# Kernel optimization log

Hardware: AMD Instinct MI355X
Metric: run time of the kernel (lower is better)

Reference implementation:

```python
import jax, jax.numpy as jnp
import numpy as np

N, E, H, C = 50000, 800000, 4, 32   # nodes, edges, heads, per-head channels
HID, LAT, G = H * C, 32, 128        # hidden, latent, num graphs
IN_DIM = 64
NEG_SLOPE = 0.2
BN_EPS = 1e-5


def setup_inputs() -> dict:
    key = jax.random.key(0)
    ks = jax.random.split(key, 20)
    inp = {
        "x": jax.random.normal(ks[0], (N, IN_DIM), jnp.float32),
        "edge_index": jax.random.randint(ks[1], (2, E), 0, N, jnp.int32),
        "batch": jnp.sort(jax.random.randint(ks[2], (N,), 0, G, jnp.int32)),
        # layer 0
        "W0": jax.random.normal(ks[3], (IN_DIM, HID), jnp.float32) * (1.0 / np.sqrt(IN_DIM)),
        "a_src0": jax.random.normal(ks[4], (H, C), jnp.float32) * 0.1,
        "a_dst0": jax.random.normal(ks[5], (H, C), jnp.float32) * 0.1,
        "b0": jnp.zeros((HID,), jnp.float32),
        # layer 1
        "W1": jax.random.normal(ks[6], (HID, HID), jnp.float32) * (1.0 / np.sqrt(HID)),
        "a_src1": jax.random.normal(ks[7], (H, C), jnp.float32) * 0.1,
        "a_dst1": jax.random.normal(ks[8], (H, C), jnp.float32) * 0.1,
        "b1": jnp.zeros((HID,), jnp.float32),
        # layer 2
        "W2": jax.random.normal(ks[9], (HID, HID), jnp.float32) * (1.0 / np.sqrt(HID)),
        "a_src2": jax.random.normal(ks[10], (H, C), jnp.float32) * 0.1,
        "a_dst2": jax.random.normal(ks[11], (H, C), jnp.float32) * 0.1,
        "b2": jnp.zeros((HID,), jnp.float32),
        # head
        "fc_w": jax.random.normal(ks[12], (HID, LAT), jnp.float32) * (1.0 / np.sqrt(HID)),
        "fc_b": jnp.zeros((LAT,), jnp.float32),
        "bn_g": jnp.ones((LAT,), jnp.float32),
        "bn_b": jnp.zeros((LAT,), jnp.float32),
    }
    return inp


def _gat_conv(x, src, dst, W, a_src, a_dst, b):
    n = x.shape[0]
    h = (x @ W).reshape(n, H, C)                      # [N,H,C]
    alpha_s = jnp.einsum("nhc,hc->nh", h, a_src)       # [N,H]
    alpha_d = jnp.einsum("nhc,hc->nh", h, a_dst)
    e = jax.nn.leaky_relu(alpha_s[src] + alpha_d[dst], NEG_SLOPE)  # [E',H]
    # scatter-softmax over incoming edges of each dst node
    m = jax.ops.segment_max(e, dst, num_segments=n)
    m = jnp.where(jnp.isfinite(m), m, 0.0)
    ex = jnp.exp(e - m[dst])
    denom = jax.ops.segment_sum(ex, dst, num_segments=n)
    alpha = ex / (denom[dst] + 1e-16)                  # [E',H]
    out = jax.ops.segment_sum(alpha[:, :, None] * h[src], dst, num_segments=n)
    return out.reshape(n, H * C) + b


def reference(x, edge_index, batch, W0, a_src0, a_dst0, b0, W1, a_src1, a_dst1, b1,
              W2, a_src2, a_dst2, b2, fc_w, fc_b, bn_g, bn_b):
    # PyG GATConv default add_self_loops=True
    loop = jnp.arange(N, dtype=edge_index.dtype)
    src = jnp.concatenate([edge_index[0], loop])
    dst = jnp.concatenate([edge_index[1], loop])

    h = x
    for (W, a_s, a_d, b) in ((W0, a_src0, a_dst0, b0),
                             (W1, a_src1, a_dst1, b1),
                             (W2, a_src2, a_dst2, b2)):
        h = _gat_conv(h, src, dst, W, a_s, a_d, b)
        h = jax.nn.leaky_relu(h, NEG_SLOPE)  # dropout is identity in eval

    pooled = jax.ops.segment_sum(h, batch, num_segments=G)  # global_add_pool -> [G,HID]
    out = pooled @ fc_w + fc_b
    # BatchNorm1d in eval mode with running_mean=0, running_var=1
    out = bn_g * out * (1.0 / np.sqrt(1.0 + BN_EPS)) + bn_b
    return out
```

## Files before the change

### kernel.cpp

```cpp
#include <hip/hip_runtime.h>
#include <hip/hip_bf16.h>
#include <float.h>

#define NEG 0.2f

__device__ __forceinline__ float leaky(float x) { return x > 0.0f ? x : NEG * x; }

__device__ __forceinline__ unsigned short f2bf(float f) {
  unsigned x = __float_as_uint(f);
  unsigned r = (x + 0x7fffu + ((x >> 16) & 1u)) >> 16;
  return (unsigned short)r;
}

__device__ __forceinline__ float2 bf2f2(unsigned u) {
  float2 r;
  r.x = __uint_as_float(u << 16);
  r.y = __uint_as_float(u & 0xffff0000u);
  return r;
}

using frag8 = __attribute__((ext_vector_type(8))) short;
using f32x4v = __attribute__((ext_vector_type(4))) float;

__global__ void zero_kernel(int* __restrict__ p, int n) {
  int i = blockIdx.x * blockDim.x + threadIdx.x;
  int stride = gridDim.x * blockDim.x;
  for (; i < n; i += stride) p[i] = 0;
}

__global__ void xcvt_kernel(const float* __restrict__ x, unsigned short* __restrict__ xb, int n) {
  int i = blockIdx.x * blockDim.x + threadIdx.x;
  if (i < n) xb[i] = f2bf(x[i]);
}

__global__ void count_kernel(const int* __restrict__ ei, int* __restrict__ deg, int E, int N) {
  int i = blockIdx.x * blockDim.x + threadIdx.x;
  if (i >= E + N) return;
  int dst = (i < E) ? ei[E + i] : (i - E);
  atomicAdd(&deg[dst], 1);
}

__global__ __launch_bounds__(1024) void scan_block_kernel(const int* __restrict__ deg,
                                                          int* __restrict__ row_start,
                                                          int* __restrict__ sums, int n) {
  __shared__ int buf[1024];
  int t = threadIdx.x;
  int idx = blockIdx.x * 1024 + t;
  int x = (idx < n) ? deg[idx] : 0;
  int v = x;
  buf[t] = v;
  __syncthreads();
  for (int off = 1; off < 1024; off <<= 1) {
    int a = (t >= off) ? buf[t - off] : 0;
    __syncthreads();
    v += a;
    buf[t] = v;
    __syncthreads();
  }
  if (idx < n) row_start[idx] = v - x;
  if (t == 1023) sums[blockIdx.x] = v;
}

__global__ __launch_bounds__(1024) void scan_sums_kernel(int* __restrict__ sums,
                                                         int* __restrict__ row_start,
                                                         int nch, int n) {
  __shared__ int buf[1024];
  int t = threadIdx.x;
  int x = (t < nch) ? sums[t] : 0;
  int v = x;
  buf[t] = v;
  __syncthreads();
  for (int off = 1; off < 1024; off <<= 1) {
    int a = (t >= off) ? buf[t - off] : 0;
    __syncthreads();
    v += a;
    buf[t] = v;
    __syncthreads();
  }
  if (t < nch) sums[t] = v - x;
  if (t == 1023) row_start[n] = v;
}

__global__ __launch_bounds__(1024) void scan_add_kernel(int* __restrict__ row_start,
                                                        const int* __restrict__ sums, int n) {
  int idx = blockIdx.x * 1024 + threadIdx.x;
  if (idx < n) row_start[idx] += sums[blockIdx.x];
}

__global__ void fill_kernel(const int* __restrict__ ei, int* __restrict__ cursor,
                            const int* __restrict__ row_start, int* __restrict__ csr_src,
                            int* __restrict__ csr_dst, int E, int N, int rpass) {
  int i = blockIdx.x * blockDim.x + threadIdx.x;
  if (i >= E + N) return;
  int src, dst;
  if (i < E) { src = ei[i]; dst = ei[E + i]; } else { src = dst = i - E; }
  if ((src >> 13) != rpass) return;
  int pos = atomicAdd(&cursor[dst], 1);
  int slot = row_start[dst] + pos;
  csr_src[slot] = src;
  csr_dst[slot] = dst;
}

__global__ __launch_bounds__(256) void gemm_kernel(const unsigned short* __restrict__ Xb,
                                                   const float* __restrict__ W,
                                                   unsigned short* __restrict__ Hb,
                                                   const float* __restrict__ a_src,
                                                   const float* __restrict__ a_dst,
                                                   float* __restrict__ as_arr,
                                                   float* __restrict__ ad_arr,
                                                   int nrows, int K) {
  __shared__ unsigned short Wt[128][136];
  __shared__ unsigned short Xs[64][136];
  int t = threadIdx.x;
  int wave = t >> 6, lane = t & 63;
  int n0 = lane & 15, quad = lane >> 4;
  int row0 = blockIdx.x * 64, wrow = wave * 16;

  for (int idx = t; idx < K * 128; idx += 256) {
    int k = idx >> 7, n = idx & 127;
    Wt[n][k] = f2bf(W[idx]);
  }
  int rowElems = K >> 3;
  for (int idx = t; idx < 64 * rowElems; idx += 256) {
    int r = idx / rowElems, c8 = idx % rowElems;
    int gr = row0 + r;
    uint4 v = make_uint4(0, 0, 0, 0);
    if (gr < nrows) v = *(const uint4*)(Xb + (size_t)gr * K + c8 * 8);
    *(uint4*)(&Xs[r][c8 * 8]) = v;
  }
  __syncthreads();

  f32x4v acc[8];
#pragma unroll
  for (int c = 0; c < 8; ++c) acc[c] = (f32x4v){0.f, 0.f, 0.f, 0.f};

  for (int kb = 0; kb < K; kb += 32) {
    frag8 a = *(const frag8*)(&Xs[wrow + n0][kb + quad * 8]);
#pragma unroll
    for (int c = 0; c < 8; ++c) {
      frag8 b = *(const frag8*)(&Wt[c * 16 + n0][kb + quad * 8]);
      acc[c] = __builtin_amdgcn_mfma_f32_16x16x32_bf16(a, b, acc[c], 0, 0, 0);
    }
  }

  float asv[8], adv[8];
#pragma unroll
  for (int c = 0; c < 8; ++c) {
    asv[c] = a_src[c * 16 + n0];
    adv[c] = a_dst[c * 16 + n0];
  }
#pragma unroll
  for (int r = 0; r < 4; ++r) {
    float ps[4] = {0.f, 0.f, 0.f, 0.f}, pd[4] = {0.f, 0.f, 0.f, 0.f};
#pragma unroll
    for (int c = 0; c < 8; ++c) {
      int h = c >> 1;
      ps[h] += acc[c][r] * asv[c];
      pd[h] += acc[c][r] * adv[c];
    }
#pragma unroll
    for (int off = 1; off < 16; off <<= 1) {
#pragma unroll
      for (int h = 0; h < 4; ++h) {
        ps[h] += __shfl_xor(ps[h], off);
        pd[h] += __shfl_xor(pd[h], off);
      }
    }
    if (n0 == 0) {
      int m = row0 + wrow + quad * 4 + r;
      if (m < nrows) {
#pragma unroll
        for (int h = 0; h < 4; ++h) {
          as_arr[(size_t)m * 4 + h] = ps[h];
          ad_arr[(size_t)m * 4 + h] = pd[h];
        }
      }
    }
  }

  __syncthreads();
#pragma unroll
  for (int c = 0; c < 8; ++c)
#pragma unroll
    for (int r = 0; r < 4; ++r)
      Xs[wrow + quad * 4 + r][c * 16 + n0] = f2bf(acc[c][r]);
  __syncthreads();
  for (int idx = t; idx < 64 * 16; idx += 256) {
    int r = idx >> 4, c8 = idx & 15;
    int gr = row0 + r;
    if (gr < nrows)
      *(uint4*)(Hb + (size_t)gr * 128 + c8 * 8) = *(const uint4*)(&Xs[r][c8 * 8]);
  }
}

__global__ __launch_bounds__(256) void ecomp_kernel(const int* __restrict__ csr_src,
                                                    const int* __restrict__ csr_dst,
                                                    const float* __restrict__ as_arr,
                                                    const float* __restrict__ ad_arr,
                                                    float* __restrict__ earr, int Etot) {
  int i = blockIdx.x * 256 + threadIdx.x;
  if (i >= Etot) return;
  int s = csr_src[i];
  int d = csr_dst[i];
  float4 a = *(const float4*)(as_arr + (size_t)s * 4);
  float4 b = *(const float4*)(ad_arr + (size_t)d * 4);
  float4 e;
  e.x = __expf(fminf(leaky(a.x + b.x), 80.f));
  e.y = __expf(fminf(leaky(a.y + b.y), 80.f));
  e.z = __expf(fminf(leaky(a.z + b.z), 80.f));
  e.w = __expf(fminf(leaky(a.w + b.w), 80.f));
  *(float4*)(earr + (size_t)i * 4) = e;
}

template <int POOL>
__global__ __launch_bounds__(256) void agg_kernel(const unsigned short* __restrict__ Hb,
                                                  const float* __restrict__ earr,
                                                  const int* __restrict__ csr_src,
                                                  const int* __restrict__ row_start,
                                                  const float* __restrict__ bias,
                                                  unsigned short* __restrict__ xnext,
                                                  const int* __restrict__ batch,
                                                  float* __restrict__ pooled, int N) {
  int wid = threadIdx.x >> 6;
  int lane = threadIdx.x & 63;
  int n = blockIdx.x * 4 + wid;
  if (n >= N) return;
  int rs = row_start[n], re = row_start[n + 1];
  int head = lane >> 4;

  const unsigned* hp = (const unsigned*)Hb + lane;
  const float* ep = earr + head;
  float denom = 0.f, acc0 = 0.f, acc1 = 0.f;
  int i = rs;
  for (; i + 4 <= re; i += 4) {
    int s0 = csr_src[i], s1 = csr_src[i + 1], s2 = csr_src[i + 2], s3 = csr_src[i + 3];
    float e0 = ep[(size_t)i * 4];
    float e1 = ep[(size_t)(i + 1) * 4];
    float e2 = ep[(size_t)(i + 2) * 4];
    float e3 = ep[(size_t)(i + 3) * 4];
    unsigned u0 = hp[(size_t)s0 * 64];
    unsigned u1 = hp[(size_t)s1 * 64];
    unsigned u2 = hp[(size_t)s2 * 64];
    unsigned u3 = hp[(size_t)s3 * 64];
    denom += (e0 + e1) + (e2 + e3);
    float2 f;
    f = bf2f2(u0); acc0 += e0 * f.x; acc1 += e0 * f.y;
    f = bf2f2(u1); acc0 += e1 * f.x; acc1 += e1 * f.y;
    f = bf2f2(u2); acc0 += e2 * f.x; acc1 += e2 * f.y;
    f = bf2f2(u3); acc0 += e3 * f.x; acc1 += e3 * f.y;
  }
  for (; i < re; ++i) {
    int s0 = csr_src[i];
    float e0 = ep[(size_t)i * 4];
    unsigned u0 = hp[(size_t)s0 * 64];
    float2 f = bf2f2(u0);
    denom += e0;
    acc0 += e0 * f.x;
    acc1 += e0 * f.y;
  }
  float inv = 1.0f / (denom + 1e-16f);
  float2 bv = *(const float2*)(bias + 2 * lane);
  float v0 = leaky(acc0 * inv + bv.x);
  float v1 = leaky(acc1 * inv + bv.y);
  if (POOL) {
    int g = batch[n];
    atomicAdd(&pooled[(size_t)g * 128 + 2 * lane], v0);
    atomicAdd(&pooled[(size_t)g * 128 + 2 * lane + 1], v1);
  } else {
    unsigned pk = ((unsigned)f2bf(v1) << 16) | (unsigned)f2bf(v0);
    ((unsigned*)xnext)[(size_t)n * 64 + lane] = pk;
  }
}

__global__ void head_kernel(const float* __restrict__ pooled, const float* __restrict__ fc_w,
                            const float* __restrict__ fc_b, const float* __restrict__ bn_g,
                            const float* __restrict__ bn_b, float* __restrict__ out, int G) {
  int t = threadIdx.x;
  int g = blockIdx.x * 8 + (t >> 5);
  int j = t & 31;
  if (g >= G) return;
  const float* pr = pooled + (size_t)g * 128;
  float acc = 0.f;
#pragma unroll 8
  for (int k = 0; k < 128; ++k) acc += pr[k] * fc_w[k * 32 + j];
  const float inv = 0.9999950000374997f;
  out[g * 32 + j] = bn_g[j] * (acc + fc_b[j]) * inv + bn_b[j];
}

extern "C" void kernel_launch(void* const* d_in, const int* in_sizes, int n_in,
                              void* d_out, int out_size, void* d_ws, size_t ws_size,
                              hipStream_t stream) {
  const float* x = (const float*)d_in[0];
  const int* ei = (const int*)d_in[1];
  const int* batch = (const int*)d_in[2];
  const float* Wm[3] = {(const float*)d_in[3], (const float*)d_in[7], (const float*)d_in[11]};
  const float* a_s[3] = {(const float*)d_in[4], (const float*)d_in[8], (const float*)d_in[12]};
  const float* a_d[3] = {(const float*)d_in[5], (const float*)d_in[9], (const float*)d_in[13]};
  const float* bb[3] = {(const float*)d_in[6], (const float*)d_in[10], (const float*)d_in[14]};
  const float* fc_w = (const float*)d_in[15];
  const float* fc_b = (const float*)d_in[16];
  const float* bn_g = (const float*)d_in[17];
  const float* bn_b = (const float*)d_in[18];
  float* out = (float*)d_out;

  int N = in_sizes[0] / 64;
  int E = in_sizes[1] / 2;
  int G = out_size / 32;
  int Etot = E + N;

  char* p = (char*)d_ws;
  auto carve = [&](size_t bytes) {
    char* r = p;
    p += (bytes + 255) & ~size_t(255);
    return r;
  };
  int* deg       = (int*)carve((size_t)N * 4);
  int* cursor    = (int*)carve((size_t)N * 4);
  float* pooled  = (float*)carve((size_t)G * 128 * 4);
  int* row_start = (int*)carve((size_t)(N + 1) * 4);
  int* sums      = (int*)carve(4096);
  int* csr_src   = (int*)carve((size_t)Etot * 4);
  int* csr_dst   = (int*)carve((size_t)Etot * 4);
  float* earr    = (float*)carve((size_t)Etot * 4 * 4);
  unsigned short* Hb = (unsigned short*)carve((size_t)N * 128 * 2);
  unsigned short* Xb = (unsigned short*)carve((size_t)N * 128 * 2);
  float* as_arr  = (float*)carve((size_t)N * 4 * 4);
  float* ad_arr  = (float*)carve((size_t)N * 4 * 4);

  int nz = (int)(((char*)(pooled + (size_t)G * 128) - (char*)deg) / 4);
  zero_kernel<<<512, 256, 0, stream>>>(deg, nz);

  xcvt_kernel<<<(N * 64 + 255) / 256, 256, 0, stream>>>(x, Xb, N * 64);

  int egrid = (Etot + 255) / 256;
  count_kernel<<<egrid, 256, 0, stream>>>(ei, deg, E, N);
  int nch = (N + 1023) / 1024;
  scan_block_kernel<<<nch, 1024, 0, stream>>>(deg, row_start, sums, N);
  scan_sums_kernel<<<1, 1024, 0, stream>>>(sums, row_start, nch, N);
  scan_add_kernel<<<nch, 1024, 0, stream>>>(row_start, sums, N);
  int npass = ((N - 1) >> 13) + 1;
  for (int r = 0; r < npass; ++r)
    fill_kernel<<<egrid, 256, 0, stream>>>(ei, cursor, row_start, csr_src, csr_dst, E, N, r);

  int ggrid = (N + 63) / 64;
  int ngrid = (N + 3) / 4;

  gemm_kernel<<<ggrid, 256, 0, stream>>>(Xb, Wm[0], Hb, a_s[0], a_d[0], as_arr, ad_arr, N, 64);
  ecomp_kernel<<<egrid, 256, 0, stream>>>(csr_src, csr_dst, as_arr, ad_arr, earr, Etot);
  agg_kernel<0><<<ngrid, 256, 0, stream>>>(Hb, earr, csr_src, row_start, bb[0],
                                           Xb, nullptr, nullptr, N);
  gemm_kernel<<<ggrid, 256, 0, stream>>>(Xb, Wm[1], Hb, a_s[1], a_d[1], as_arr, ad_arr, N, 128);
  ecomp_kernel<<<egrid, 256, 0, stream>>>(csr_src, csr_dst, as_arr, ad_arr, earr, Etot);
  agg_kernel<0><<<ngrid, 256, 0, stream>>>(Hb, earr, csr_src, row_start, bb[1],
                                           Xb, nullptr, nullptr, N);
  gemm_kernel<<<ggrid, 256, 0, stream>>>(Xb, Wm[2], Hb, a_s[2], a_d[2], as_arr, ad_arr, N, 128);
  ecomp_kernel<<<egrid, 256, 0, stream>>>(csr_src, csr_dst, as_arr, ad_arr, earr, Etot);
  agg_kernel<1><<<ngrid, 256, 0, stream>>>(Hb, earr, csr_src, row_start, bb[2],
                                           nullptr, batch, pooled, N);

  head_kernel<<<(G + 7) / 8, 256, 0, stream>>>(pooled, fc_w, fc_b, bn_g, bn_b, out, G);
}
```

Baseline: 495.9 us.

## Replace multi-pass CSR fill with per-(dst,src-segment) bucket counts in one pass

Degree counting now happens per (destination, source-segment) bucket, and the prefix scan runs over N*nseg buckets. This lets the CSR fill finish in a single pass while keeping edges within each row sorted by source segment, which previously took one full edge pass per segment. The aggregation kernel reads row bounds from the segmented offsets. In exchange the scan and count arrays grow by a factor of nseg (7), and bucket atomics spread more widely.

Result: faster. 472.8 us (-4.7%).

```diff
diff --git a/kernel.cpp b/kernel.cpp
--- a/kernel.cpp
+++ b/kernel.cpp
@@ -3,6 +3,7 @@
 #include <float.h>
 
 #define NEG 0.2f
+#define SEGSHIFT 13
 
 __device__ __forceinline__ float leaky(float x) { return x > 0.0f ? x : NEG * x; }
 
@@ -33,11 +34,13 @@
   if (i < n) xb[i] = f2bf(x[i]);
 }
 
-__global__ void count_kernel(const int* __restrict__ ei, int* __restrict__ deg, int E, int N) {
+__global__ void count_kernel(const int* __restrict__ ei, int* __restrict__ degseg,
+                             int E, int N, int nseg) {
   int i = blockIdx.x * blockDim.x + threadIdx.x;
   if (i >= E + N) return;
-  int dst = (i < E) ? ei[E + i] : (i - E);
-  atomicAdd(&deg[dst], 1);
+  int src, dst;
+  if (i < E) { src = ei[i]; dst = ei[E + i]; } else { src = dst = i - E; }
+  atomicAdd(&degseg[(size_t)dst * nseg + (src >> SEGSHIFT)], 1);
 }
 
 __global__ __launch_bounds__(1024) void scan_block_kernel(const int* __restrict__ deg,
@@ -88,15 +91,15 @@
 }
 
 __global__ void fill_kernel(const int* __restrict__ ei, int* __restrict__ cursor,
-                            const int* __restrict__ row_start, int* __restrict__ csr_src,
-                            int* __restrict__ csr_dst, int E, int N, int rpass) {
+                            const int* __restrict__ rowseg, int* __restrict__ csr_src,
+                            int* __restrict__ csr_dst, int E, int N, int nseg) {
   int i = blockIdx.x * blockDim.x + threadIdx.x;
   if (i >= E + N) return;
   int src, dst;
   if (i < E) { src = ei[i]; dst = ei[E + i]; } else { src = dst = i - E; }
-  if ((src >> 13) != rpass) return;
-  int pos = atomicAdd(&cursor[dst], 1);
-  int slot = row_start[dst] + pos;
+  size_t b = (size_t)dst * nseg + (src >> SEGSHIFT);
+  int pos = atomicAdd(&cursor[b], 1);
+  int slot = rowseg[b] + pos;
   csr_src[slot] = src;
   csr_dst[slot] = dst;
 }
@@ -216,16 +219,18 @@
 __global__ __launch_bounds__(256) void agg_kernel(const unsigned short* __restrict__ Hb,
                                                   const float* __restrict__ earr,
                                                   const int* __restrict__ csr_src,
-                                                  const int* __restrict__ row_start,
+                                                  const int* __restrict__ rowseg,
                                                   const float* __restrict__ bias,
                                                   unsigned short* __restrict__ xnext,
                                                   const int* __restrict__ batch,
-                                                  float* __restrict__ pooled, int N) {
+                                                  float* __restrict__ pooled,
+                                                  int N, int nseg) {
   int wid = threadIdx.x >> 6;
   int lane = threadIdx.x & 63;
   int n = blockIdx.x * 4 + wid;
   if (n >= N) return;
-  int rs = row_start[n], re = row_start[n + 1];
+  int rs = rowseg[(size_t)n * nseg];
+  int re = rowseg[(size_t)n * nseg + nseg];
   int head = lane >> 4;
 
   const unsigned* hp = (const unsigned*)Hb + lane;
@@ -307,6 +312,8 @@
   int E = in_sizes[1] / 2;
   int G = out_size / 32;
   int Etot = E + N;
+  int nseg = ((N - 1) >> SEGSHIFT) + 1;
+  int L = N * nseg;
 
   char* p = (char*)d_ws;
   auto carve = [&](size_t bytes) {
@@ -314,10 +321,10 @@
     p += (bytes + 255) & ~size_t(255);
     return r;
   };
-  int* deg       = (int*)carve((size_t)N * 4);
-  int* cursor    = (int*)carve((size_t)N * 4);
+  int* degseg    = (int*)carve((size_t)L * 4);
+  int* cursor    = (int*)carve((size_t)L * 4);
   float* pooled  = (float*)carve((size_t)G * 128 * 4);
-  int* row_start = (int*)carve((size_t)(N + 1) * 4);
+  int* rowseg    = (int*)carve((size_t)(L + 1) * 4);
   int* sums      = (int*)carve(4096);
   int* csr_src   = (int*)carve((size_t)Etot * 4);
   int* csr_dst   = (int*)carve((size_t)Etot * 4);
@@ -327,36 +334,34 @@
   float* as_arr  = (float*)carve((size_t)N * 4 * 4);
   float* ad_arr  = (float*)carve((size_t)N * 4 * 4);
 
-  int nz = (int)(((char*)(pooled + (size_t)G * 128) - (char*)deg) / 4);
-  zero_kernel<<<512, 256, 0, stream>>>(deg, nz);
+  int nz = (int)(((char*)(pooled + (size_t)G * 128) - (char*)degseg) / 4);
+  zero_kernel<<<512, 256, 0, stream>>>(degseg, nz);
 
   xcvt_kernel<<<(N * 64 + 255) / 256, 256, 0, stream>>>(x, Xb, N * 64);
 
   int egrid = (Etot + 255) / 256;
-  count_kernel<<<egrid, 256, 0, stream>>>(ei, deg, E, N);
-  int nch = (N + 1023) / 1024;
-  scan_block_kernel<<<nch, 1024, 0, stream>>>(deg, row_start, sums, N);
-  scan_sums_kernel<<<1, 1024, 0, stream>>>(sums, row_start, nch, N);
-  scan_add_kernel<<<nch, 1024, 0, stream>>>(row_start, sums, N);
-  int npass = ((N - 1) >> 13) + 1;
-  for (int r = 0; r < npass; ++r)
-    fill_kernel<<<egrid, 256, 0, stream>>>(ei, cursor, row_start, csr_src, csr_dst, E, N, r);
+  count_kernel<<<egrid, 256, 0, stream>>>(ei, degseg, E, N, nseg);
+  int nch = (L + 1023) / 1024;
+  scan_block_kernel<<<nch, 1024, 0, stream>>>(degseg, rowseg, sums, L);
+  scan_sums_kernel<<<1, 1024, 0, stream>>>(sums, rowseg, nch, L);
+  scan_add_kernel<<<nch, 1024, 0, stream>>>(rowseg, sums, L);
+  fill_kernel<<<egrid, 256, 0, stream>>>(ei, cursor, rowseg, csr_src, csr_dst, E, N, nseg);
 
   int ggrid = (N + 63) / 64;
   int ngrid = (N + 3) / 4;
 
   gemm_kernel<<<ggrid, 256, 0, stream>>>(Xb, Wm[0], Hb, a_s[0], a_d[0], as_arr, ad_arr, N, 64);
   ecomp_kernel<<<egrid, 256, 0, stream>>>(csr_src, csr_dst, as_arr, ad_arr, earr, Etot);
-  agg_kernel<0><<<ngrid, 256, 0, stream>>>(Hb, earr, csr_src, row_start, bb[0],
-                                           Xb, nullptr, nullptr, N);
+  agg_kernel<0><<<ngrid, 256, 0, stream>>>(Hb, earr, csr_src, rowseg, bb[0],
+                                           Xb, nullptr, nullptr, N, nseg);
   gemm_kernel<<<ggrid, 256, 0, stream>>>(Xb, Wm[1], Hb, a_s[1], a_d[1], as_arr, ad_arr, N, 128);
   ecomp_kernel<<<egrid, 256, 0, stream>>>(csr_src, csr_dst, as_arr, ad_arr, earr, Etot);
-  agg_kernel<0><<<ngrid, 256, 0, stream>>>(Hb, earr, csr_src, row_start, bb[1],
-                                           Xb, nullptr, nullptr, N);
+  agg_kernel<0><<<ngrid, 256, 0, stream>>>(Hb, earr, csr_src, rowseg, bb[1],
+                                           Xb, nullptr, nullptr, N, nseg);
   gemm_kernel<<<ggrid, 256, 0, stream>>>(Xb, Wm[2], Hb, a_s[2], a_d[2], as_arr, ad_arr, N, 128);
   ecomp_kernel<<<egrid, 256, 0, stream>>>(csr_src, csr_dst, as_arr, ad_arr, earr, Etot);
-  agg_kernel<1><<<ngrid, 256, 0, stream>>>(Hb, earr, csr_src, row_start, bb[2],
-                                           nullptr, batch, pooled, N);
+  agg_kernel<1><<<ngrid, 256, 0, stream>>>(Hb, earr, csr_src, rowseg, bb[2],
+                                           nullptr, batch, pooled, N, nseg);
 
   head_kernel<<<(G + 7) / 8, 256, 0, stream>>>(pooled, fc_w, fc_b, bn_g, bn_b, out, G);
 }
```
